# Kernel optimization log

Hardware: AMD Instinct MI355X
Metric: run time of the kernel (lower is better)

## Reference

```python
import jax, jax.numpy as jnp
import numpy as np
from jax import lax

BN_EPS = 1e-5


def _zpool(x, axis):
    # stack (mean, max) over `axis` as 2 channels -> [N, 2, A, B]
    return jnp.stack([jnp.mean(x, axis=axis), jnp.max(x, axis=axis)], axis=1)


def _gate(p2, conv_w, conv_b, bn_w, bn_b, bn_rm, bn_rv, i):
    # p2: [N, 2, A, B]; 7x7 conv (2->1, pad 3) + scalar BN + relu + sigmoid
    y = lax.conv_general_dilated(
        p2, conv_w, window_strides=(1, 1), padding=[(3, 3), (3, 3)],
        dimension_numbers=("NCHW", "OIHW", "NCHW"))[:, 0] + conv_b[0]  # [N, A, B]
    y = (y - bn_rm[i]) * lax.rsqrt(bn_rv[i] + BN_EPS) * bn_w[i] + bn_b[i]
    return jax.nn.sigmoid(jnp.maximum(y, 0.0))


def setup_inputs() -> dict:
    key = jax.random.key(0)
    ks = jax.random.split(key, 7)
    N, C, H, W = 256, 2048, 7, 7
    return {
        "x": jax.random.normal(ks[0], (N, C, H, W), dtype=jnp.float32),
        "conv_w": jax.random.normal(ks[1], (1, 2, 7, 7), dtype=jnp.float32) * 0.1,
        "conv_b": jax.random.normal(ks[2], (1,), dtype=jnp.float32) * 0.1,
        "bn_w": jax.random.normal(ks[3], (3,), dtype=jnp.float32),
        "bn_b": jax.random.normal(ks[4], (3,), dtype=jnp.float32),
        "bn_rm": jax.random.normal(ks[5], (3,), dtype=jnp.float32) * 0.1,
        "bn_rv": jax.random.uniform(ks[6], (3,), dtype=jnp.float32),
    }


def reference(x, conv_w, conv_b, bn_w, bn_b, bn_rm, bn_rv):
    # x: [N, C, 7, 7]
    g_hw = _gate(_zpool(x, 1), conv_w, conv_b, bn_w, bn_b, bn_rm, bn_rv, 0)  # [N, 7, 7]
    g_ch = _gate(_zpool(x, 3), conv_w, conv_b, bn_w, bn_b, bn_rm, bn_rv, 1)  # [N, C, 7] indexed by h
    g_cw = _gate(_zpool(x, 2), conv_w, conv_b, bn_w, bn_b, bn_rm, bn_rv, 2)  # [N, C, 7] indexed by w
    gate = (g_hw[:, None, :, :] + g_ch[:, :, :, None] + g_cw[:, :, None, :]) * (1.0 / 3.0)
    return x * gate
```

## Files before the change

kernel.cpp:

```cpp
#include <hip/hip_runtime.h>

#define N_ 256
#define C_ 2048
#define HW_ 49
#define CPB 64
#define NCC 32
#define NCHUNK 8

#define CHB(lc) ((lc) * HW_ + ((lc) >= 3 ? 1 : 0))

__global__ __launch_bounds__(256) void k_poolc(const float* __restrict__ x,
                                               float* __restrict__ psum,
                                               float* __restrict__ pmax) {
  const int bc = blockIdx.x, n = blockIdx.y;
  const int t = threadIdx.x;
  __shared__ __align__(16) float sx[CPB * HW_];
  __shared__ float part_s[HW_][5];
  __shared__ float part_m[HW_][5];

  float sm = 0.f, mx = -3.4e38f;
  const int hw = t / 5, s = t % 5;

  const float4* xv = (const float4*)(x + ((size_t)n * C_ + (size_t)bc * 256) * HW_);
  #pragma unroll
  for (int pass = 0; pass < 4; ++pass) {
    float4* sv = (float4*)sx;
    for (int v = t; v < 784; v += 256) sv[v] = xv[pass * 784 + v];
    __syncthreads();
    if (t < 245) {
      #pragma unroll
      for (int j = 0; j < 13; ++j) {
        int c = s * 13 + j;
        if (c < CPB) {
          float a = sx[c * HW_ + hw];
          sm += a; mx = fmaxf(mx, a);
        }
      }
    }
    __syncthreads();
  }
  if (t < 245) { part_s[hw][s] = sm; part_m[hw][s] = mx; }
  __syncthreads();
  if (t < HW_) {
    float s2 = 0.f, m2 = -3.4e38f;
    #pragma unroll
    for (int k = 0; k < 5; ++k) { s2 += part_s[t][k]; m2 = fmaxf(m2, part_m[t][k]); }
    size_t o = ((size_t)n * NCHUNK + bc) * HW_ + t;
    psum[o] = s2; pmax[o] = m2;
  }
}

__global__ __launch_bounds__(64) void k_ghw(const float* __restrict__ psum,
                                            const float* __restrict__ pmax,
                                            const float* __restrict__ cw,
                                            const float* __restrict__ cb,
                                            const float* __restrict__ bnw,
                                            const float* __restrict__ bnb,
                                            const float* __restrict__ bnrm,
                                            const float* __restrict__ bnrv,
                                            float* __restrict__ ghw) {
  const int n = blockIdx.x;
  const int t = threadIdx.x;
  __shared__ float p2c[2][13][13];
  __shared__ float s_cw[98];

  for (int i = t; i < 2 * 13 * 13; i += 64) ((float*)p2c)[i] = 0.f;
  for (int i = t; i < 98; i += 64) s_cw[i] = cw[i];
  __syncthreads();

  if (t < HW_) {
    float sm = 0.f, mx = -3.4e38f;
    const float* ps = psum + (size_t)n * NCHUNK * HW_ + t;
    const float* pm = pmax + (size_t)n * NCHUNK * HW_ + t;
    #pragma unroll
    for (int cc = 0; cc < NCHUNK; ++cc) {
      sm += ps[cc * HW_];
      mx = fmaxf(mx, pm[cc * HW_]);
    }
    p2c[0][t / 7 + 3][t % 7 + 3] = sm * (1.f / C_);
    p2c[1][t / 7 + 3][t % 7 + 3] = mx;
  }
  __syncthreads();

  if (t < HW_) {
    int a = t / 7, b = t % 7;
    float y = cb[0];
    #pragma unroll
    for (int i2 = 0; i2 < 2; ++i2)
      #pragma unroll
      for (int p = 0; p < 7; ++p)
        #pragma unroll
        for (int q = 0; q < 7; ++q)
          y += p2c[i2][a + p][b + q] * s_cw[i2 * 49 + p * 7 + q];
    float sc = bnw[0] * rsqrtf(bnrv[0] + 1e-5f);
    y = (y - bnrm[0]) * sc + bnb[0];
    y = fmaxf(y, 0.f);
    ghw[n * HW_ + t] = 1.f / (1.f + __expf(-y));
  }
}

__global__ __launch_bounds__(256, 6) void k_main(const float* __restrict__ x,
    const float* __restrict__ ghw,
    const float* __restrict__ cw, const float* __restrict__ cb,
    const float* __restrict__ bnw, const float* __restrict__ bnb,
    const float* __restrict__ bnrm, const float* __restrict__ bnrv,
    float* __restrict__ out) {
  const int cc = blockIdx.x;
  const int n  = (N_ - 1) - blockIdx.y;
  const int c0 = cc * CPB;
  const int t  = threadIdx.x;

  __shared__ __align__(16) float sx[3432];
  __shared__ __align__(16) float pool_lo[1120];
  __shared__ __align__(16) float pool_hi[1120];
  __shared__ float gch[448];
  __shared__ float gcw[448];
  __shared__ __align__(16) float s_w[112];
  __shared__ float s_ghw[49];

  const int conv = t & 1, i2 = (t >> 1) & 1, cl = t >> 2;
  const int bi = 1 + conv;
  const float cb0 = cb[0];
  const float sc_bn = bnw[bi] * rsqrtf(bnrv[bi] + 1e-5f);
  const float rm_bn = bnrm[bi];
  const float sh_bn = bnb[bi];

  if (t < 112) {
    int i2w = t / 56, rem = t % 56, p = rem / 8, q = rem % 8;
    s_w[t] = (q < 7) ? cw[i2w * 49 + p * 7 + q] : 0.f;
  }
  if (t < HW_) s_ghw[t] = ghw[n * HW_ + t];
  for (int i = t; i < 2 * 3 * HW_; i += 256) {
    int side = i / 147, off = i % 147;
    int lc = side ? (67 + off / HW_) : (off / HW_);
    int c = c0 - 3 + lc;
    float vv = 0.f;
    if (c >= 0 && c < C_) vv = x[((size_t)n * C_ + c) * HW_ + off % HW_];
    sx[CHB(lc) + off % HW_] = vv;
  }
  const float4* xv = (const float4*)(x + ((size_t)n * C_ + c0) * HW_);
  float4* sxv = (float4*)(sx + 148);
  for (int v = t; v < 784; v += 256) sxv[v] = xv[v];
  __syncthreads();

  for (int i = t; i < 70 * 7; i += 256) {
    int lc = i / 7, k = i % 7;
    int base = CHB(lc);
    float s1 = 0.f, m1 = -3.4e38f, s2 = 0.f, m2 = -3.4e38f;
    #pragma unroll
    for (int j = 0; j < 7; ++j) {
      float a = sx[base + k * 7 + j];
      s1 += a; m1 = fmaxf(m1, a);
      float b = sx[base + j * 7 + k];
      s2 += b; m2 = fmaxf(m2, b);
    }
    float* pb = (k < 4) ? pool_lo : pool_hi;
    int kk = k & 3;
    pb[(0 * 70 + lc) * 4 + kk] = s1 * (1.f / 7.f);
    pb[(1 * 70 + lc) * 4 + kk] = m1;
    pb[(2 * 70 + lc) * 4 + kk] = s2 * (1.f / 7.f);
    pb[(3 * 70 + lc) * 4 + kk] = m2;
  }
  __syncthreads();

  {
    const int f = conv * 2 + i2;
    const float* Wb = s_w + i2 * 56;
    float acc[7] = {0.f, 0.f, 0.f, 0.f, 0.f, 0.f, 0.f};
    #pragma unroll
    for (int p = 0; p < 7; ++p) {
      int ri = (f * 70 + cl + p) * 4;
      float4 r0 = *(const float4*)(pool_lo + ri);
      float4 r1 = *(const float4*)(pool_hi + ri);
      float row[7] = {r0.x, r0.y, r0.z, r0.w, r1.x, r1.y, r1.z};
      float4 w0 = *(const float4*)(Wb + p * 8);
      float4 w1 = *(const float4*)(Wb + p * 8 + 4);
      float wr[7] = {w0.x, w0.y, w0.z, w0.w, w1.x, w1.y, w1.z};
      #pragma unroll
      for (int q = 0; q < 7; ++q) {
        #pragma unroll
        for (int k = 0; k < 7; ++k) {
          int c = k + q - 3;
          if (c >= 0 && c < 7) acc[k] += row[c] * wr[q];
        }
      }
    }
    float fsum[7];
    #pragma unroll
    for (int k = 0; k < 7; ++k) fsum[k] = acc[k] + __shfl_xor(acc[k], 2, 64);
    if (i2 == 0) {
      float* gp = (conv ? gcw : gch) + cl * 7;
      #pragma unroll
      for (int k = 0; k < 7; ++k) {
        float y = (fsum[k] + cb0 - rm_bn) * sc_bn + sh_bn;
        y = fmaxf(y, 0.f);
        gp[k] = 1.f / (1.f + __expf(-y));
      }
    }
  }
  __syncthreads();

  float4* outv = (float4*)(out + ((size_t)n * C_ + c0) * HW_);
  for (int v = t; v < 784; v += 256) {
    float4 q = sxv[v];
    int e0 = v * 4;
    int cj = e0 / 49;
    int hw0 = e0 - cj * 49;
    float r0 = q.x, r1 = q.y, r2 = q.z, r3 = q.w;
    {
      int hw = hw0;
      int cjj = cj + (hw >= 49); hw -= (hw >= 49) ? 49 : 0;
      int h = (hw * 37) >> 8, w2 = hw - h * 7;
      r0 *= (s_ghw[hw] + gch[cjj * 7 + h] + gcw[cjj * 7 + w2]) * (1.f / 3.f);
    }
    {
      int hw = hw0 + 1;
      int cjj = cj + (hw >= 49); hw -= (hw >= 49) ? 49 : 0;
      int h = (hw * 37) >> 8, w2 = hw - h * 7;
      r1 *= (s_ghw[hw] + gch[cjj * 7 + h] + gcw[cjj * 7 + w2]) * (1.f / 3.f);
    }
    {
      int hw = hw0 + 2;
      int cjj = cj + (hw >= 49); hw -= (hw >= 49) ? 49 : 0;
      int h = (hw * 37) >> 8, w2 = hw - h * 7;
      r2 *= (s_ghw[hw] + gch[cjj * 7 + h] + gcw[cjj * 7 + w2]) * (1.f / 3.f);
    }
    {
      int hw = hw0 + 3;
      int cjj = cj + (hw >= 49); hw -= (hw >= 49) ? 49 : 0;
      int h = (hw * 37) >> 8, w2 = hw - h * 7;
      r3 *= (s_ghw[hw] + gch[cjj * 7 + h] + gcw[cjj * 7 + w2]) * (1.f / 3.f);
    }
    outv[v] = make_float4(r0, r1, r2, r3);
  }
}

extern "C" void kernel_launch(void* const* d_in, const int* in_sizes, int n_in,
                              void* d_out, int out_size, void* d_ws, size_t ws_size,
                              hipStream_t stream) {
  const float* x    = (const float*)d_in[0];
  const float* cw   = (const float*)d_in[1];
  const float* cb   = (const float*)d_in[2];
  const float* bnw  = (const float*)d_in[3];
  const float* bnb  = (const float*)d_in[4];
  const float* bnrm = (const float*)d_in[5];
  const float* bnrv = (const float*)d_in[6];
  float* out = (float*)d_out;

  float* psum = (float*)d_ws;
  float* pmax = psum + (size_t)N_ * NCHUNK * HW_;
  float* ghw  = pmax + (size_t)N_ * NCHUNK * HW_;

  k_poolc<<<dim3(NCHUNK, N_), 256, 0, stream>>>(x, psum, pmax);
  k_ghw<<<dim3(N_), 64, 0, stream>>>(psum, pmax, cw, cb, bnw, bnb, bnrm, bnrv, ghw);
  k_main<<<dim3(NCC, N_), 256, 0, stream>>>(x, ghw, cw, cb, bnw, bnb, bnrm, bnrv, out);
}
```

Measured before the change: 79.03 us.

## Make main kernel persistent over four channel chunks with register-prefetched double buffering

Each block of the main kernel now handles four consecutive 64-channel chunks instead of one, cutting the grid from 32 to 8 blocks per sample. The next chunk's interior and halo are loaded into registers at the start of each iteration, then written into a second shared buffer after the conv step, so global loads overlap with pooling and gate compute. In exchange, shared memory per block roughly doubles, the occupancy hint drops from 6 to 4 blocks per CU, and fewer total blocks are available to hide latency.

```diff
diff --git a/kernel.cpp b/kernel.cpp
--- a/kernel.cpp
+++ b/kernel.cpp
@@ -4,7 +4,6 @@
 #define C_ 2048
 #define HW_ 49
 #define CPB 64
-#define NCC 32
 #define NCHUNK 8
 
 #define CHB(lc) ((lc) * HW_ + ((lc) >= 3 ? 1 : 0))
@@ -31,10 +30,7 @@
       #pragma unroll
       for (int j = 0; j < 13; ++j) {
         int c = s * 13 + j;
-        if (c < CPB) {
-          float a = sx[c * HW_ + hw];
-          sm += a; mx = fmaxf(mx, a);
-        }
+        if (c < CPB) { float a = sx[c * HW_ + hw]; sm += a; mx = fmaxf(mx, a); }
       }
     }
     __syncthreads();
@@ -99,18 +95,17 @@
   }
 }
 
-__global__ __launch_bounds__(256, 6) void k_main(const float* __restrict__ x,
+__global__ __launch_bounds__(256, 4) void k_main_p(const float* __restrict__ x,
     const float* __restrict__ ghw,
     const float* __restrict__ cw, const float* __restrict__ cb,
     const float* __restrict__ bnw, const float* __restrict__ bnb,
     const float* __restrict__ bnrm, const float* __restrict__ bnrv,
     float* __restrict__ out) {
-  const int cc = blockIdx.x;
+  const int bx = blockIdx.x;
   const int n  = (N_ - 1) - blockIdx.y;
-  const int c0 = cc * CPB;
   const int t  = threadIdx.x;
 
-  __shared__ __align__(16) float sx[3432];
+  __shared__ __align__(16) float sx[2][3432];
   __shared__ __align__(16) float pool_lo[1120];
   __shared__ __align__(16) float pool_hi[1120];
   __shared__ float gch[448];
@@ -130,108 +125,129 @@
     s_w[t] = (q < 7) ? cw[i2w * 49 + p * 7 + q] : 0.f;
   }
   if (t < HW_) s_ghw[t] = ghw[n * HW_ + t];
-  for (int i = t; i < 2 * 3 * HW_; i += 256) {
-    int side = i / 147, off = i % 147;
-    int lc = side ? (67 + off / HW_) : (off / HW_);
-    int c = c0 - 3 + lc;
-    float vv = 0.f;
-    if (c >= 0 && c < C_) vv = x[((size_t)n * C_ + c) * HW_ + off % HW_];
-    sx[CHB(lc) + off % HW_] = vv;
-  }
-  const float4* xv = (const float4*)(x + ((size_t)n * C_ + c0) * HW_);
-  float4* sxv = (float4*)(sx + 148);
-  for (int v = t; v < 784; v += 256) sxv[v] = xv[v];
-  __syncthreads();
-
-  for (int i = t; i < 70 * 7; i += 256) {
-    int lc = i / 7, k = i % 7;
-    int base = CHB(lc);
-    float s1 = 0.f, m1 = -3.4e38f, s2 = 0.f, m2 = -3.4e38f;
-    #pragma unroll
-    for (int j = 0; j < 7; ++j) {
-      float a = sx[base + k * 7 + j];
-      s1 += a; m1 = fmaxf(m1, a);
-      float b = sx[base + j * 7 + k];
-      s2 += b; m2 = fmaxf(m2, b);
-    }
-    float* pb = (k < 4) ? pool_lo : pool_hi;
-    int kk = k & 3;
-    pb[(0 * 70 + lc) * 4 + kk] = s1 * (1.f / 7.f);
-    pb[(1 * 70 + lc) * 4 + kk] = m1;
-    pb[(2 * 70 + lc) * 4 + kk] = s2 * (1.f / 7.f);
-    pb[(3 * 70 + lc) * 4 + kk] = m2;
-  }
-  __syncthreads();
-
   {
-    const int f = conv * 2 + i2;
-    const float* Wb = s_w + i2 * 56;
-    float acc[7] = {0.f, 0.f, 0.f, 0.f, 0.f, 0.f, 0.f};
-    #pragma unroll
-    for (int p = 0; p < 7; ++p) {
-      int ri = (f * 70 + cl + p) * 4;
-      float4 r0 = *(const float4*)(pool_lo + ri);
-      float4 r1 = *(const float4*)(pool_hi + ri);
-      float row[7] = {r0.x, r0.y, r0.z, r0.w, r1.x, r1.y, r1.z};
-      float4 w0 = *(const float4*)(Wb + p * 8);
-      float4 w1 = *(const float4*)(Wb + p * 8 + 4);
-      float wr[7] = {w0.x, w0.y, w0.z, w0.w, w1.x, w1.y, w1.z};
-      #pragma unroll
-      for (int q = 0; q < 7; ++q) {
+    const int c0 = (bx * 4) * CPB;
+    for (int i = t; i < 294; i += 256) {
+      int side = i / 147, off = i % 147;
+      int lc = side ? (67 + off / HW_) : (off / HW_);
+      int c = c0 - 3 + lc;
+      float vv = 0.f;
+      if (c >= 0 && c < C_) vv = x[((size_t)n * C_ + c) * HW_ + off % HW_];
+      sx[0][CHB(lc) + off % HW_] = vv;
+    }
+    const float4* xv = (const float4*)(x + ((size_t)n * C_ + c0) * HW_);
+    float4* sxv = (float4*)(&sx[0][148]);
+    for (int v = t; v < 784; v += 256) sxv[v] = xv[v];
+  }
+  __syncthreads();
+
+  #pragma unroll
+  for (int j = 0; j < 4; ++j) {
+    const int cur = j & 1, nxt = cur ^ 1;
+    const int cc = bx * 4 + j;
+    const int c0 = cc * CPB;
+    float* sxc = sx[cur];
+
+    float4 q0, q1, q2, q3;
+    float h0, h1;
+    if (j < 3) {
+      const int c0n = (cc + 1) * CPB;
+      const float4* xvn = (const float4*)(x + ((size_t)n * C_ + c0n) * HW_);
+      if (t < 196) { q0 = xvn[t]; q1 = xvn[t + 196]; q2 = xvn[t + 392]; q3 = xvn[t + 588]; }
+      if (t < 147) {
+        int lcl = t / 49, off = t % 49;
+        int cl_ = c0n - 3 + lcl;
+        int ch_ = c0n + CPB + lcl;
+        h0 = (cl_ >= 0 && cl_ < C_) ? x[((size_t)n * C_ + cl_) * HW_ + off] : 0.f;
+        h1 = (ch_ < C_) ? x[((size_t)n * C_ + ch_) * HW_ + off] : 0.f;
+      }
+    }
+
+    for (int i = t; i < 70 * 7; i += 256) {
+      int lc = i / 7, k = i % 7;
+      int base = CHB(lc);
+      float s1 = 0.f, m1 = -3.4e38f, s2 = 0.f, m2 = -3.4e38f;
+      #pragma unroll
+      for (int jj = 0; jj < 7; ++jj) {
+        float a = sxc[base + k * 7 + jj]; s1 += a; m1 = fmaxf(m1, a);
+        float b = sxc[base + jj * 7 + k]; s2 += b; m2 = fmaxf(m2, b);
+      }
+      float* pb = (k < 4) ? pool_lo : pool_hi;
+      int kk = k & 3;
+      pb[(0 * 70 + lc) * 4 + kk] = s1 * (1.f / 7.f);
+      pb[(1 * 70 + lc) * 4 + kk] = m1;
+      pb[(2 * 70 + lc) * 4 + kk] = s2 * (1.f / 7.f);
+      pb[(3 * 70 + lc) * 4 + kk] = m2;
+    }
+    __syncthreads();
+
+    {
+      const int f = conv * 2 + i2;
+      const float* Wb = s_w + i2 * 56;
+      float acc[7] = {0.f, 0.f, 0.f, 0.f, 0.f, 0.f, 0.f};
+      #pragma unroll
+      for (int p = 0; p < 7; ++p) {
+        int ri = (f * 70 + cl + p) * 4;
+        float4 r0 = *(const float4*)(pool_lo + ri);
+        float4 r1 = *(const float4*)(pool_hi + ri);
+        float row[7] = {r0.x, r0.y, r0.z, r0.w, r1.x, r1.y, r1.z};
+        float4 w0 = *(const float4*)(Wb + p * 8);
+        float4 w1 = *(const float4*)(Wb + p * 8 + 4);
+        float wr[7] = {w0.x, w0.y, w0.z, w0.w, w1.x, w1.y, w1.z};
+        #pragma unroll
+        for (int q = 0; q < 7; ++q)
+          #pragma unroll
+          for (int k = 0; k < 7; ++k) {
+            int c = k + q - 3;
+            if (c >= 0 && c < 7) acc[k] += row[c] * wr[q];
+          }
+      }
+      float fsum[7];
+      #pragma unroll
+      for (int k = 0; k < 7; ++k) fsum[k] = acc[k] + __shfl_xor(acc[k], 2, 64);
+      if (i2 == 0) {
+        float* gp = (conv ? gcw : gch) + cl * 7;
         #pragma unroll
         for (int k = 0; k < 7; ++k) {
-          int c = k + q - 3;
-          if (c >= 0 && c < 7) acc[k] += row[c] * wr[q];
+          float y = (fsum[k] + cb0 - rm_bn) * sc_bn + sh_bn;
+          y = fmaxf(y, 0.f);
+          gp[k] = 1.f / (1.f + __expf(-y));
         }
       }
     }
-    float fsum[7];
-    #pragma unroll
-    for (int k = 0; k < 7; ++k) fsum[k] = acc[k] + __shfl_xor(acc[k], 2, 64);
-    if (i2 == 0) {
-      float* gp = (conv ? gcw : gch) + cl * 7;
-      #pragma unroll
-      for (int k = 0; k < 7; ++k) {
-        float y = (fsum[k] + cb0 - rm_bn) * sc_bn + sh_bn;
-        y = fmaxf(y, 0.f);
-        gp[k] = 1.f / (1.f + __expf(-y));
-      }
-    }
-  }
-  __syncthreads();
-
-  float4* outv = (float4*)(out + ((size_t)n * C_ + c0) * HW_);
-  for (int v = t; v < 784; v += 256) {
-    float4 q = sxv[v];
-    int e0 = v * 4;
-    int cj = e0 / 49;
-    int hw0 = e0 - cj * 49;
-    float r0 = q.x, r1 = q.y, r2 = q.z, r3 = q.w;
+
+    if (j < 3) {
+      float* sxn = sx[nxt];
+      float4* sxnv = (float4*)(sxn + 148);
+      if (t < 196) { sxnv[t] = q0; sxnv[t + 196] = q1; sxnv[t + 392] = q2; sxnv[t + 588] = q3; }
+      if (t < 147) {
+        int lcl = t / 49, off = t % 49;
+        sxn[CHB(lcl) + off] = h0;
+        sxn[CHB(67 + lcl) + off] = h1;
+      }
+    }
+    __syncthreads();
+
     {
-      int hw = hw0;
-      int cjj = cj + (hw >= 49); hw -= (hw >= 49) ? 49 : 0;
-      int h = (hw * 37) >> 8, w2 = hw - h * 7;
-      r0 *= (s_ghw[hw] + gch[cjj * 7 + h] + gcw[cjj * 7 + w2]) * (1.f / 3.f);
-    }
-    {
-      int hw = hw0 + 1;
-      int cjj = cj + (hw >= 49); hw -= (hw >= 49) ? 49 : 0;
-      int h = (hw * 37) >> 8, w2 = hw - h * 7;
-      r1 *= (s_ghw[hw] + gch[cjj * 7 + h] + gcw[cjj * 7 + w2]) * (1.f / 3.f);
-    }
-    {
-      int hw = hw0 + 2;
-      int cjj = cj + (hw >= 49); hw -= (hw >= 49) ? 49 : 0;
-      int h = (hw * 37) >> 8, w2 = hw - h * 7;
-      r2 *= (s_ghw[hw] + gch[cjj * 7 + h] + gcw[cjj * 7 + w2]) * (1.f / 3.f);
-    }
-    {
-      int hw = hw0 + 3;
-      int cjj = cj + (hw >= 49); hw -= (hw >= 49) ? 49 : 0;
-      int h = (hw * 37) >> 8, w2 = hw - h * 7;
-      r3 *= (s_ghw[hw] + gch[cjj * 7 + h] + gcw[cjj * 7 + w2]) * (1.f / 3.f);
-    }
-    outv[v] = make_float4(r0, r1, r2, r3);
+      const float4* sxv = (const float4*)(sxc + 148);
+      float4* outv = (float4*)(out + ((size_t)n * C_ + c0) * HW_);
+      for (int v = t; v < 784; v += 256) {
+        float4 q = sxv[v];
+        int e0 = v * 4;
+        int cj = e0 / 49;
+        int hw0 = e0 - cj * 49;
+        float r[4] = {q.x, q.y, q.z, q.w};
+        #pragma unroll
+        for (int jj = 0; jj < 4; ++jj) {
+          int hw = hw0 + jj;
+          int cjj = cj + (hw >= 49);
+          hw -= (hw >= 49) ? 49 : 0;
+          int h = (hw * 37) >> 8, w2 = hw - h * 7;
+          r[jj] *= (s_ghw[hw] + gch[cjj * 7 + h] + gcw[cjj * 7 + w2]) * (1.f / 3.f);
+        }
+        outv[v] = make_float4(r[0], r[1], r[2], r[3]);
+      }
+    }
   }
 }
 
@@ -253,5 +269,6 @@
 
   k_poolc<<<dim3(NCHUNK, N_), 256, 0, stream>>>(x, psum, pmax);
   k_ghw<<<dim3(N_), 64, 0, stream>>>(psum, pmax, cw, cb, bnw, bnb, bnrm, bnrv, ghw);
-  k_main<<<dim3(NCC, N_), 256, 0, stream>>>(x, ghw, cw, cb, bnw, bnb, bnrm, bnrv, out);
-}
+  k_main_p<<<dim3(NCHUNK, N_), 256, 0, stream>>>(x, ghw, cw, cb, bnw, bnb, bnrm,
+                                                 bnrv, out);
+}
```

New measurement: 76.96 us, median of 2. 1.03x faster.
